# Optimization experiments

Measured on AMD Instinct MI355X. Metric: run time of the kernel, lower is better.

Reference implementation:

```python
import jax, jax.numpy as jnp
import numpy as np

INPUT_SIZE = 8
HIDDEN = 12
N_ACTIONS = 4
B, T = 4096, 1024


def setup_inputs() -> dict:
    key = jax.random.key(0)
    ks = jax.random.split(key, 7)
    s_ih = 1.0 / np.sqrt(HIDDEN)
    # PyTorch LSTM params: W_ih [4H, I], W_hh [4H, H], b_ih [4H], b_hh [4H]; gate order i,f,g,o
    return {
        "x": jax.random.normal(ks[0], (B, T, INPUT_SIZE), dtype=jnp.float32),
        "W_ih": jax.random.uniform(ks[1], (4 * HIDDEN, INPUT_SIZE), jnp.float32, -s_ih, s_ih),
        "W_hh": jax.random.uniform(ks[2], (4 * HIDDEN, HIDDEN), jnp.float32, -s_ih, s_ih),
        "b_ih": jax.random.uniform(ks[3], (4 * HIDDEN,), jnp.float32, -s_ih, s_ih),
        "b_hh": jax.random.uniform(ks[4], (4 * HIDDEN,), jnp.float32, -s_ih, s_ih),
        "W_fc": jax.random.uniform(ks[5], (N_ACTIONS, HIDDEN), jnp.float32, -s_ih, s_ih),
        "b_fc": jax.random.uniform(ks[6], (N_ACTIONS,), jnp.float32, -s_ih, s_ih),
    }


def _lstm(x, W_ih, W_hh, b_ih, b_hh):
    # x: [B, T, I]. Precompute input contribution for all timesteps (one big GEMM).
    xW = jnp.einsum("bti,gi->tbg", x, W_ih) + (b_ih + b_hh)  # [T, B, 4H]
    Bsz = x.shape[0]
    h0 = jnp.zeros((Bsz, HIDDEN), x.dtype)
    c0 = jnp.zeros((Bsz, HIDDEN), x.dtype)

    def step(carry, xw_t):
        h, c = carry
        gates = xw_t + h @ W_hh.T  # [B, 4H]
        i, f, g, o = jnp.split(gates, 4, axis=-1)  # PyTorch gate order i,f,g,o
        i = jax.nn.sigmoid(i)
        f = jax.nn.sigmoid(f)
        g = jnp.tanh(g)
        o = jax.nn.sigmoid(o)
        c = f * c + i * g
        h = o * jnp.tanh(c)
        return (h, c), h

    (hn, cn), hs = jax.lax.scan(step, (h0, c0), xW)
    return jnp.swapaxes(hs, 0, 1), hn, cn  # hs -> [B, T, H]


def reference(x, W_ih, W_hh, b_ih, b_hh, W_fc, b_fc):
    hs, hn, cn = _lstm(x, W_ih, W_hh, b_ih, b_hh)
    out = hs @ W_fc.T + b_fc  # [B, T, n_actions]
    # match torch: hn/cn have leading num_layers dim (=1)
    return out, (hn[None], cn[None])
```

## Files before the change

kernel.cpp:

```cpp
#include <hip/hip_runtime.h>
#include <cstddef>
#include <cstdint>

namespace {

typedef __fp16 h2v __attribute__((ext_vector_type(2)));

constexpr int kB = 4096, kT = 1024, kI = 8, kH = 12, kA = 4;
constexpr int kTC  = 32;
constexpr int kNCH = kT / kTC;
constexpr int kXRegU = 132;
constexpr int kBlkU  = 16 * kXRegU;

constexpr float kL2E  = 1.442695041f;
constexpr float kL2E2 = 2.885390082f;

template<int N>
__device__ __forceinline__ uint32_t ror16u(uint32_t v) {
    return (uint32_t)__builtin_amdgcn_mov_dpp((int)v, 0x120 + N, 0xF, 0xF, false);
}
__device__ __forceinline__ float ror16f1(float v) {
    return __int_as_float(__builtin_amdgcn_mov_dpp(__float_as_int(v), 0x121, 0xF, 0xF, false));
}
__device__ __forceinline__ uint32_t pkrtz(float lo, float hi) {
    auto v = __builtin_amdgcn_cvt_pkrtz(lo, hi);
    return __builtin_bit_cast(uint32_t, v);
}
__device__ __forceinline__ h2v uh(uint32_t u) { return __builtin_bit_cast(h2v, u); }

__global__ __launch_bounds__(256, 1)
void lstm_fused_kernel(const float* __restrict__ x,
                       const float* __restrict__ W_ih,
                       const float* __restrict__ W_hh,
                       const float* __restrict__ b_ih,
                       const float* __restrict__ b_hh,
                       const float* __restrict__ W_fc,
                       const float* __restrict__ b_fc,
                       float* __restrict__ out) {
    __shared__ uint32_t xs[2][kBlkU];

    const int tid = threadIdx.x;
    const int wv  = tid >> 6;
    const int l64 = tid & 63;
    const int grp = l64 >> 4;
    const int r   = l64 & 15;
    const int ei  = wv * 4 + grp;
    const int b   = blockIdx.x * 16 + ei;
    const bool isFC = (r >= kH);
    const int a   = isFC ? (r - kH) : 0;

    const int probe = __builtin_amdgcn_mov_dpp(r, 0x121, 0xF, 0xF, false);
    const int dir   = (probe - r) & 15;

    h2v wp[4][8], xp[4][4];
    float bs[4];
    if (!isFC) {
#pragma unroll
        for (int g = 0; g < 4; ++g) {
            const int row = g * kH + r;
            const float scl = (g == 2) ? -kL2E2 : -kL2E;
#pragma unroll
            for (int jj = 0; jj < 8; ++jj) {
                const int c0 = (r + dir * 2 * jj) & 15;
                const int c1 = (c0 + dir) & 15;
                const float u0 = (c0 < kH) ? W_hh[row * kH + c0] : 0.0f;
                const float u1 = (c1 < kH) ? W_hh[row * kH + c1] : 0.0f;
                wp[g][jj] = h2v{(__fp16)(scl * u0), (__fp16)(scl * u1)};
            }
#pragma unroll
            for (int i2 = 0; i2 < 4; ++i2)
                xp[g][i2] = h2v{(__fp16)(scl * W_ih[row * kI + 2 * i2]),
                                (__fp16)(scl * W_ih[row * kI + 2 * i2 + 1])};
            bs[g] = scl * (b_ih[row] + b_hh[row]);
        }
    } else {
#pragma unroll
        for (int jj = 0; jj < 8; ++jj) {
            const int c0 = (r + dir * 2 * jj) & 15;
            const int c1 = (c0 + dir) & 15;
            const float u0 = (c0 < kH) ? W_fc[a * kH + c0] : 0.0f;
            const float u1 = (c1 < kH) ? W_fc[a * kH + c1] : 0.0f;
            wp[0][jj] = h2v{(__fp16)u0, (__fp16)u1};
            wp[1][jj] = h2v{(__fp16)0.f, (__fp16)0.f};
            wp[2][jj] = wp[1][jj];
            wp[3][jj] = wp[1][jj];
        }
#pragma unroll
        for (int i2 = 0; i2 < 4; ++i2) {
            xp[0][i2] = h2v{(__fp16)0.f, (__fp16)0.f};
            xp[1][i2] = xp[0][i2]; xp[2][i2] = xp[0][i2]; xp[3][i2] = xp[0][i2];
        }
        bs[0] = b_fc[a]; bs[1] = 0.0f; bs[2] = 0.0f; bs[3] = 0.0f;
    }

    const float* xg = x + (size_t)b * (kT * kI);
    const int reg = ei * kXRegU;

    float4 rv0, rv1, rv2, rv3;
    {
        const float4* gp = (const float4*)xg;
        rv0 = gp[r]; rv1 = gp[16 + r]; rv2 = gp[32 + r]; rv3 = gp[48 + r];
        uint2 u;
        u.x = pkrtz(rv0.x, rv0.y); u.y = pkrtz(rv0.z, rv0.w);
        *(uint2*)&xs[0][reg + 2 * r] = u;
        u.x = pkrtz(rv1.x, rv1.y); u.y = pkrtz(rv1.z, rv1.w);
        *(uint2*)&xs[0][reg + 32 + 2 * r] = u;
        u.x = pkrtz(rv2.x, rv2.y); u.y = pkrtz(rv2.z, rv2.w);
        *(uint2*)&xs[0][reg + 64 + 2 * r] = u;
        u.x = pkrtz(rv3.x, rv3.y); u.y = pkrtz(rv3.z, rv3.w);
        *(uint2*)&xs[0][reg + 96 + 2 * r] = u;
    }
    asm volatile("s_waitcnt lgkmcnt(0)" ::: "memory");
    __builtin_amdgcn_sched_barrier(0);
    uint4 xr = *(const uint4*)&xs[0][reg];

    float h = 0.0f, c = 0.0f;
    uint32_t hrp[8];
#pragma unroll
    for (int k = 0; k < 8; ++k) hrp[k] = 0u;

    float* op = out + (size_t)b * (kT * kA) + a;

    int cb = 0;
#pragma unroll 1
    for (int ch = 0; ch < kNCH; ++ch) {
        if (ch + 1 < kNCH) {
            const float4* gp = (const float4*)(xg + (size_t)(ch + 1) * (kTC * kI));
            rv0 = gp[r]; rv1 = gp[16 + r]; rv2 = gp[32 + r]; rv3 = gp[48 + r];
        }
#pragma unroll 2
        for (int tt = 0; tt < kTC; ++tt) {
            uint4 xrn;
            if (tt + 1 < kTC) xrn = *(const uint4*)&xs[cb][reg + (tt + 1) * 4];
            float s0 = bs[0], s1 = bs[1], s2 = bs[2], s3 = bs[3];
#pragma unroll
            for (int jj = 0; jj < 8; ++jj) {
                const h2v hv = uh(hrp[jj]);
                s0 = __builtin_amdgcn_fdot2(wp[0][jj], hv, s0, false);
                s1 = __builtin_amdgcn_fdot2(wp[1][jj], hv, s1, false);
                s2 = __builtin_amdgcn_fdot2(wp[2][jj], hv, s2, false);
                s3 = __builtin_amdgcn_fdot2(wp[3][jj], hv, s3, false);
            }
            {
                const h2v xv0 = uh(xr.x), xv1 = uh(xr.y), xv2 = uh(xr.z), xv3 = uh(xr.w);
                s0 = __builtin_amdgcn_fdot2(xp[0][0], xv0, s0, false);
                s1 = __builtin_amdgcn_fdot2(xp[1][0], xv0, s1, false);
                s2 = __builtin_amdgcn_fdot2(xp[2][0], xv0, s2, false);
                s3 = __builtin_amdgcn_fdot2(xp[3][0], xv0, s3, false);
                s0 = __builtin_amdgcn_fdot2(xp[0][1], xv1, s0, false);
                s1 = __builtin_amdgcn_fdot2(xp[1][1], xv1, s1, false);
                s2 = __builtin_amdgcn_fdot2(xp[2][1], xv1, s2, false);
                s3 = __builtin_amdgcn_fdot2(xp[3][1], xv1, s3, false);
                s0 = __builtin_amdgcn_fdot2(xp[0][2], xv2, s0, false);
                s1 = __builtin_amdgcn_fdot2(xp[1][2], xv2, s1, false);
                s2 = __builtin_amdgcn_fdot2(xp[2][2], xv2, s2, false);
                s3 = __builtin_amdgcn_fdot2(xp[3][2], xv2, s3, false);
                s0 = __builtin_amdgcn_fdot2(xp[0][3], xv3, s0, false);
                s1 = __builtin_amdgcn_fdot2(xp[1][3], xv3, s1, false);
                s2 = __builtin_amdgcn_fdot2(xp[2][3], xv3, s2, false);
                s3 = __builtin_amdgcn_fdot2(xp[3][3], xv3, s3, false);
            }
            if ((ch | tt) != 0) { if (isFC) op[-kA] = s0; }
            const float iv = __builtin_amdgcn_rcpf(1.0f + __builtin_amdgcn_exp2f(s0));
            const float fv = __builtin_amdgcn_rcpf(1.0f + __builtin_amdgcn_exp2f(s1));
            const float gv = fmaf(2.0f, __builtin_amdgcn_rcpf(1.0f + __builtin_amdgcn_exp2f(s2)), -1.0f);
            const float ov = __builtin_amdgcn_rcpf(1.0f + __builtin_amdgcn_exp2f(s3));
            c = fmaf(fv, c, iv * gv);
            const float ec = __builtin_amdgcn_exp2f(-kL2E2 * c);
            const float tc = fmaf(2.0f, __builtin_amdgcn_rcpf(1.0f + ec), -1.0f);
            h = ov * tc;
            const float hn1 = ror16f1(h);
            const uint32_t Q = pkrtz(h, hn1);
            hrp[0] = Q;
            hrp[1] = ror16u<2>(Q);
            hrp[2] = ror16u<4>(Q);
            hrp[3] = ror16u<6>(Q);
            hrp[4] = ror16u<8>(Q);
            hrp[5] = ror16u<10>(Q);
            hrp[6] = ror16u<12>(Q);
            hrp[7] = ror16u<14>(Q);
            if (tt + 1 < kTC) xr = xrn;
            op += kA;
        }
        if (ch + 1 < kNCH) {
            const int nb = cb ^ 1;
            uint2 u;
            u.x = pkrtz(rv0.x, rv0.y); u.y = pkrtz(rv0.z, rv0.w);
            *(uint2*)&xs[nb][reg + 2 * r] = u;
            u.x = pkrtz(rv1.x, rv1.y); u.y = pkrtz(rv1.z, rv1.w);
            *(uint2*)&xs[nb][reg + 32 + 2 * r] = u;
            u.x = pkrtz(rv2.x, rv2.y); u.y = pkrtz(rv2.z, rv2.w);
            *(uint2*)&xs[nb][reg + 64 + 2 * r] = u;
            u.x = pkrtz(rv3.x, rv3.y); u.y = pkrtz(rv3.z, rv3.w);
            *(uint2*)&xs[nb][reg + 96 + 2 * r] = u;
            asm volatile("s_waitcnt lgkmcnt(0)" ::: "memory");
            __builtin_amdgcn_sched_barrier(0);
            xr = *(const uint4*)&xs[nb][reg];
            cb = nb;
        }
    }

    {
        float s0 = bs[0];
#pragma unroll
        for (int jj = 0; jj < 8; ++jj)
            s0 = __builtin_amdgcn_fdot2(wp[0][jj], uh(hrp[jj]), s0, false);
        if (isFC) op[-kA] = s0;
    }
    if (!isFC) {
        float* hn = out + (size_t)kB * kT * kA;
        hn[(size_t)b * kH + r] = h;
        hn[(size_t)kB * kH + (size_t)b * kH + r] = c;
    }
}

}

extern "C" void kernel_launch(void* const* d_in, const int* in_sizes, int n_in,
                              void* d_out, int out_size, void* d_ws, size_t ws_size,
                              hipStream_t stream) {
    (void)in_sizes; (void)n_in; (void)d_ws; (void)ws_size; (void)out_size;
    const float* x    = (const float*)d_in[0];
    const float* W_ih = (const float*)d_in[1];
    const float* W_hh = (const float*)d_in[2];
    const float* b_ih = (const float*)d_in[3];
    const float* b_hh = (const float*)d_in[4];
    const float* W_fc = (const float*)d_in[5];
    const float* b_fc = (const float*)d_in[6];
    float* out = (float*)d_out;
    hipLaunchKernelGGL(lstm_fused_kernel, dim3(kB / 16), dim3(256), 0, stream,
                       x, W_ih, W_hh, b_ih, b_hh, W_fc, b_fc, out);
}
```

Before: 246.7 us.

## Precompute next-step input projection off the critical path and split recurrent dot chain

Moves the x·W_ih dot products for step t+1 so they are computed during step t, after the gates, and carries the result in registers. The per-step serial chain then holds only the recurrent h·W_hh terms. That chain is split into two independent accumulator chains (jj 0-3 and 4-7) that are summed at the end, shortening the dependent fdot2 latency. The cost is extra live registers and one extra add per gate.

```diff
diff --git a/kernel.cpp b/kernel.cpp
--- a/kernel.cpp
+++ b/kernel.cpp
@@ -23,10 +23,15 @@
     return __int_as_float(__builtin_amdgcn_mov_dpp(__float_as_int(v), 0x121, 0xF, 0xF, false));
 }
 __device__ __forceinline__ uint32_t pkrtz(float lo, float hi) {
-    auto v = __builtin_amdgcn_cvt_pkrtz(lo, hi);
-    return __builtin_bit_cast(uint32_t, v);
+    return __builtin_bit_cast(uint32_t, __builtin_amdgcn_cvt_pkrtz(lo, hi));
 }
 __device__ __forceinline__ h2v uh(uint32_t u) { return __builtin_bit_cast(h2v, u); }
+__device__ __forceinline__ float fd2(h2v w, h2v v, float acc) {
+    return __builtin_amdgcn_fdot2(w, v, acc, false);
+}
+__device__ __forceinline__ float sigf(float s) {
+    return __builtin_amdgcn_rcpf(1.0f + __builtin_amdgcn_exp2f(s));
+}
 
 __global__ __launch_bounds__(256, 1)
 void lstm_fused_kernel(const float* __restrict__ x,
@@ -112,12 +117,21 @@
     }
     asm volatile("s_waitcnt lgkmcnt(0)" ::: "memory");
     __builtin_amdgcn_sched_barrier(0);
-    uint4 xr = *(const uint4*)&xs[0][reg];
 
     float h = 0.0f, c = 0.0f;
     uint32_t hrp[8];
 #pragma unroll
     for (int k = 0; k < 8; ++k) hrp[k] = 0u;
+
+    float xq0, xq1, xq2, xq3;
+    {
+        const uint4 x0 = *(const uint4*)&xs[0][reg];
+        const h2v v0 = uh(x0.x), v1 = uh(x0.y), v2 = uh(x0.z), v3 = uh(x0.w);
+        xq0 = fd2(xp[0][3], v3, fd2(xp[0][2], v2, fd2(xp[0][1], v1, fd2(xp[0][0], v0, bs[0]))));
+        xq1 = fd2(xp[1][3], v3, fd2(xp[1][2], v2, fd2(xp[1][1], v1, fd2(xp[1][0], v0, bs[1]))));
+        xq2 = fd2(xp[2][3], v3, fd2(xp[2][2], v2, fd2(xp[2][1], v1, fd2(xp[2][0], v0, bs[2]))));
+        xq3 = fd2(xp[3][3], v3, fd2(xp[3][2], v2, fd2(xp[3][1], v1, fd2(xp[3][0], v0, bs[3]))));
+    }
 
     float* op = out + (size_t)b * (kT * kA) + a;
 
@@ -130,44 +144,52 @@
         }
 #pragma unroll 2
         for (int tt = 0; tt < kTC; ++tt) {
-            uint4 xrn;
-            if (tt + 1 < kTC) xrn = *(const uint4*)&xs[cb][reg + (tt + 1) * 4];
-            float s0 = bs[0], s1 = bs[1], s2 = bs[2], s3 = bs[3];
-#pragma unroll
-            for (int jj = 0; jj < 8; ++jj) {
+            uint4 xn;
+            if (tt + 1 < kTC) xn = *(const uint4*)&xs[cb][reg + (tt + 1) * 4];
+            float a0 = xq0, a1 = xq1, a2 = xq2, a3 = xq3;
+            float e0, e1, e2, e3;
+            {
+                const h2v h4 = uh(hrp[4]);
+                e0 = fd2(wp[0][4], h4, 0.0f);
+                e1 = fd2(wp[1][4], h4, 0.0f);
+                e2 = fd2(wp[2][4], h4, 0.0f);
+                e3 = fd2(wp[3][4], h4, 0.0f);
+            }
+#pragma unroll
+            for (int jj = 0; jj < 4; ++jj) {
                 const h2v hv = uh(hrp[jj]);
-                s0 = __builtin_amdgcn_fdot2(wp[0][jj], hv, s0, false);
-                s1 = __builtin_amdgcn_fdot2(wp[1][jj], hv, s1, false);
-                s2 = __builtin_amdgcn_fdot2(wp[2][jj], hv, s2, false);
-                s3 = __builtin_amdgcn_fdot2(wp[3][jj], hv, s3, false);
-            }
-            {
-                const h2v xv0 = uh(xr.x), xv1 = uh(xr.y), xv2 = uh(xr.z), xv3 = uh(xr.w);
-                s0 = __builtin_amdgcn_fdot2(xp[0][0], xv0, s0, false);
-                s1 = __builtin_amdgcn_fdot2(xp[1][0], xv0, s1, false);
-                s2 = __builtin_amdgcn_fdot2(xp[2][0], xv0, s2, false);
-                s3 = __builtin_amdgcn_fdot2(xp[3][0], xv0, s3, false);
-                s0 = __builtin_amdgcn_fdot2(xp[0][1], xv1, s0, false);
-                s1 = __builtin_amdgcn_fdot2(xp[1][1], xv1, s1, false);
-                s2 = __builtin_amdgcn_fdot2(xp[2][1], xv1, s2, false);
-                s3 = __builtin_amdgcn_fdot2(xp[3][1], xv1, s3, false);
-                s0 = __builtin_amdgcn_fdot2(xp[0][2], xv2, s0, false);
-                s1 = __builtin_amdgcn_fdot2(xp[1][2], xv2, s1, false);
-                s2 = __builtin_amdgcn_fdot2(xp[2][2], xv2, s2, false);
-                s3 = __builtin_amdgcn_fdot2(xp[3][2], xv2, s3, false);
-                s0 = __builtin_amdgcn_fdot2(xp[0][3], xv3, s0, false);
-                s1 = __builtin_amdgcn_fdot2(xp[1][3], xv3, s1, false);
-                s2 = __builtin_amdgcn_fdot2(xp[2][3], xv3, s2, false);
-                s3 = __builtin_amdgcn_fdot2(xp[3][3], xv3, s3, false);
-            }
+                a0 = fd2(wp[0][jj], hv, a0);
+                a1 = fd2(wp[1][jj], hv, a1);
+                a2 = fd2(wp[2][jj], hv, a2);
+                a3 = fd2(wp[3][jj], hv, a3);
+            }
+#pragma unroll
+            for (int jj = 5; jj < 8; ++jj) {
+                const h2v hv = uh(hrp[jj]);
+                e0 = fd2(wp[0][jj], hv, e0);
+                e1 = fd2(wp[1][jj], hv, e1);
+                e2 = fd2(wp[2][jj], hv, e2);
+                e3 = fd2(wp[3][jj], hv, e3);
+            }
+            const float s0 = a0 + e0;
+            const float s1 = a1 + e1;
+            const float s2 = a2 + e2;
+            const float s3 = a3 + e3;
             if ((ch | tt) != 0) { if (isFC) op[-kA] = s0; }
-            const float iv = __builtin_amdgcn_rcpf(1.0f + __builtin_amdgcn_exp2f(s0));
-            const float fv = __builtin_amdgcn_rcpf(1.0f + __builtin_amdgcn_exp2f(s1));
-            const float gv = fmaf(2.0f, __builtin_amdgcn_rcpf(1.0f + __builtin_amdgcn_exp2f(s2)), -1.0f);
-            const float ov = __builtin_amdgcn_rcpf(1.0f + __builtin_amdgcn_exp2f(s3));
+            const float iv = sigf(s0);
+            const float fv = sigf(s1);
+            const float gv = fmaf(2.0f, sigf(s2), -1.0f);
+            const float ov = sigf(s3);
+            float n0, n1, n2, n3;
+            if (tt + 1 < kTC) {
+                const h2v v0 = uh(xn.x), v1 = uh(xn.y), v2 = uh(xn.z), v3 = uh(xn.w);
+                n0 = fd2(xp[0][3], v3, fd2(xp[0][2], v2, fd2(xp[0][1], v1, fd2(xp[0][0], v0, bs[0]))));
+                n1 = fd2(xp[1][3], v3, fd2(xp[1][2], v2, fd2(xp[1][1], v1, fd2(xp[1][0], v0, bs[1]))));
+                n2 = fd2(xp[2][3], v3, fd2(xp[2][2], v2, fd2(xp[2][1], v1, fd2(xp[2][0], v0, bs[2]))));
+                n3 = fd2(xp[3][3], v3, fd2(xp[3][2], v2, fd2(xp[3][1], v1, fd2(xp[3][0], v0, bs[3]))));
+            }
             c = fmaf(fv, c, iv * gv);
-            const float ec = __builtin_amdgcn_exp2f(-kL2E2 * c);
-            const float tc = fmaf(2.0f, __builtin_amdgcn_rcpf(1.0f + ec), -1.0f);
+            const float tc = fmaf(2.0f, sigf(-kL2E2 * c), -1.0f);
             h = ov * tc;
             const float hn1 = ror16f1(h);
             const uint32_t Q = pkrtz(h, hn1);
@@ -179,7 +201,7 @@
             hrp[5] = ror16u<10>(Q);
             hrp[6] = ror16u<12>(Q);
             hrp[7] = ror16u<14>(Q);
-            if (tt + 1 < kTC) xr = xrn;
+            if (tt + 1 < kTC) { xq0 = n0; xq1 = n1; xq2 = n2; xq3 = n3; }
             op += kA;
         }
         if (ch + 1 < kNCH) {
@@ -195,7 +217,14 @@
             *(uint2*)&xs[nb][reg + 96 + 2 * r] = u;
             asm volatile("s_waitcnt lgkmcnt(0)" ::: "memory");
             __builtin_amdgcn_sched_barrier(0);
-            xr = *(const uint4*)&xs[nb][reg];
+            {
+                const uint4 x0 = *(const uint4*)&xs[nb][reg];
+                const h2v v0 = uh(x0.x), v1 = uh(x0.y), v2 = uh(x0.z), v3 = uh(x0.w);
+                xq0 = fd2(xp[0][3], v3, fd2(xp[0][2], v2, fd2(xp[0][1], v1, fd2(xp[0][0], v0, bs[0]))));
+                xq1 = fd2(xp[1][3], v3, fd2(xp[1][2], v2, fd2(xp[1][1], v1, fd2(xp[1][0], v0, bs[1]))));
+                xq2 = fd2(xp[2][3], v3, fd2(xp[2][2], v2, fd2(xp[2][1], v1, fd2(xp[2][0], v0, bs[2]))));
+                xq3 = fd2(xp[3][3], v3, fd2(xp[3][2], v2, fd2(xp[3][1], v1, fd2(xp[3][0], v0, bs[3]))));
+            }
             cb = nb;
         }
     }
@@ -204,7 +233,7 @@
         float s0 = bs[0];
 #pragma unroll
         for (int jj = 0; jj < 8; ++jj)
-            s0 = __builtin_amdgcn_fdot2(wp[0][jj], uh(hrp[jj]), s0, false);
+            s0 = fd2(wp[0][jj], uh(hrp[jj]), s0);
         if (isFC) op[-kA] = s0;
     }
     if (!isFC) {
```

After: 298.9 us. 21.1% more time.
